# Kernel tuning notes

Measured on AMD Instinct MI355X. Metric: run time of the kernel, lower is better.

The kernel has to match this reference:

```python
import jax, jax.numpy as jnp
import numpy as np

N = 100000
D = 256
E = 300000


def setup_inputs() -> dict:
    key = jax.random.key(0)
    ks = jax.random.split(key, 9)
    x_all = jax.random.normal(ks[0], (N, D), dtype=jnp.float32)
    edge_index = jax.random.randint(ks[1], (2, E), 0, N, dtype=jnp.int64)
    s = 1.0 / np.sqrt(D)
    params = {}
    for i, layer in enumerate(["1", "2", "3"]):
        params[f"Wl{layer}"] = jax.random.uniform(ks[2 + 2 * i], (D, D), jnp.float32, -s, s)
        params[f"Wr{layer}"] = jax.random.uniform(ks[3 + 2 * i], (D, D), jnp.float32, -s, s)
        params[f"b{layer}"] = jnp.zeros((D,), jnp.float32)
    return {"edge_index": edge_index, "x_all": x_all, **params}


def sage_conv(x, src, dst, Wl, Wr, b):
    # PyG SAGEConv: lin_l(mean_{j in N(i)} x_j) + lin_r(x_i), bias on lin_l
    msgs = x[src]                                        # [E, D] gather
    agg = jax.ops.segment_sum(msgs, dst, num_segments=N)  # [N, D]
    deg = jax.ops.segment_sum(jnp.ones((src.shape[0],), x.dtype), dst, num_segments=N)
    agg = agg / jnp.maximum(deg, 1.0)[:, None]           # mean; isolated nodes -> 0
    return agg @ Wl.T + x @ Wr.T + b


def reference(edge_index, x_all, Wl1, Wr1, b1, Wl2, Wr2, b2, Wl3, Wr3, b3):
    src, dst = edge_index[0], edge_index[1]
    x = jax.nn.relu(sage_conv(x_all, src, dst, Wl1, Wr1, b1))
    # dropout p=0.4 is identity at inference (training=False)
    x = jax.nn.relu(sage_conv(x, src, dst, Wl2, Wr2, b2))
    x = sage_conv(x, src, dst, Wl3, Wr3, b3)
    return x
```

## Files before the change

kernel.cpp:

```cpp
#include <hip/hip_runtime.h>

typedef unsigned short ushort_t;
typedef unsigned int   u32;
typedef __attribute__((ext_vector_type(8))) short bf16x8;
typedef __attribute__((ext_vector_type(4))) float f32x4;

#define NNODES 100000
#define DIM    256
#define NEDGE  300000
#define KTOT   512
#define KSTEPS 16
#define BROWS  128
#define NTILES 16
#define WCT    8
#define SLICE  16384


__global__ void count_kernel(const int* __restrict__ dst, int* __restrict__ cnt, int E) {
    int e = blockIdx.x * blockDim.x + threadIdx.x;
    if (e < E) atomicAdd(&cnt[dst[e]], 1);
}

__global__ void scan1(const int* __restrict__ cnt, int* __restrict__ partial, int n) {
    __shared__ int s[256];
    int i = blockIdx.x * 256 + threadIdx.x;
    s[threadIdx.x] = (i < n) ? cnt[i] : 0;
    __syncthreads();
    for (int off = 128; off > 0; off >>= 1) {
        if (threadIdx.x < off) s[threadIdx.x] += s[threadIdx.x + off];
        __syncthreads();
    }
    if (threadIdx.x == 0) partial[blockIdx.x] = s[0];
}

__global__ void scan2(int* __restrict__ partial, int nb) {
    __shared__ int s[512];
    int t = threadIdx.x;
    int orig = (t < nb) ? partial[t] : 0;
    s[t] = orig;
    __syncthreads();
    for (int off = 1; off < 512; off <<= 1) {
        int v = (t >= off) ? s[t - off] : 0;
        __syncthreads();
        s[t] += v;
        __syncthreads();
    }
    if (t < nb) partial[t] = s[t] - orig;
}

__global__ void scan3(const int* __restrict__ cnt, const int* __restrict__ partial,
                      int* __restrict__ row_start, int n) {
    __shared__ int s[256];
    int i = blockIdx.x * 256 + threadIdx.x;
    int v = (i < n) ? cnt[i] : 0;
    s[threadIdx.x] = v;
    __syncthreads();
    for (int off = 1; off < 256; off <<= 1) {
        int t = (threadIdx.x >= off) ? s[threadIdx.x - off] : 0;
        __syncthreads();
        s[threadIdx.x] += t;
        __syncthreads();
    }
    if (i < n) row_start[i] = partial[blockIdx.x] + s[threadIdx.x] - v;
}

__global__ void fill_csr(const int* __restrict__ src, const int* __restrict__ dst,
                         const int* __restrict__ row_start, int* __restrict__ cursor,
                         int* __restrict__ esrc, int E) {
    int e = blockIdx.x * blockDim.x + threadIdx.x;
    if (e < E) {
        int d = dst[e];
        int pos = row_start[d] + atomicAdd(&cursor[d], 1);
        esrc[pos] = src[e];
    }
}

__global__ __launch_bounds__(256) void aggregate(
    const int* __restrict__ esrc, const int* __restrict__ row_start,
    const int* __restrict__ cnt, const float* __restrict__ x, float* __restrict__ agg)
{
    int node = (blockIdx.x * blockDim.x + threadIdx.x) >> 6;
    int lane = threadIdx.x & 63;
    if (node >= NNODES) return;
    int start = row_start[node];
    int c = cnt[node];
    float4 acc = make_float4(0.f, 0.f, 0.f, 0.f);
    for (int i = 0; i < c; i++) {
        int s = esrc[start + i];
        float4 v = ((const float4*)(x + (size_t)s * DIM))[lane];
        acc.x += v.x; acc.y += v.y; acc.z += v.z; acc.w += v.w;
    }
    float inv = (c > 0) ? 1.0f / (float)c : 0.0f;
    ((float4*)(agg + (size_t)node * DIM))[lane] =
        make_float4(acc.x * inv, acc.y * inv, acc.z * inv, acc.w * inv);
}

__global__ void conv_weights(const float* __restrict__ Wl, const float* __restrict__ Wr,
                             ushort_t* __restrict__ Bsw) {
    int idx = blockIdx.x * 256 + threadIdx.x;
    if (idx >= 256 * KTOT) return;
    int n = idx >> 9, k = idx & 511;
    float v = (k < DIM) ? Wl[n * DIM + k] : Wr[n * DIM + (k - DIM)];
    unsigned u = __float_as_uint(v);
    unsigned hb = u & 0xFFFF0000u;
    float lo = v - __uint_as_float(hb);
    int ks = k >> 5, q = (k >> 3) & 3, j = k & 7;
    int ct = n >> 4, nn = n & 15;
    int base = ks * SLICE + ct * 512 + q * 128 + nn * 8 + j;
    Bsw[base]        = (ushort_t)(u >> 16);
    Bsw[base + 8192] = (ushort_t)(__float_as_uint(lo) >> 16);
}


__device__ __forceinline__ void stage_b_async(const ushort_t* __restrict__ slice,
                                              ushort_t* buf, int tid) {
    const int wave = tid >> 6;
    #pragma unroll
    for (int i = 0; i < 4; i++) {
        const int c  = tid + i * 512;
        const int cb = wave * 64 + i * 512;
        __builtin_amdgcn_global_load_lds(
            (const __attribute__((address_space(1))) u32*)(slice + (size_t)c * 8),
            (__attribute__((address_space(3))) u32*)(buf + cb * 8),
            16, 0, 0);
    }
}

__device__ __forceinline__ void load_a(const float* __restrict__ base, int row0, int row1,
                                       int kk, int M, float* va ) {
    if (row0 < M) {
        *(float4*)(va + 0) = *(const float4*)(base + (size_t)row0 * DIM + kk);
        *(float4*)(va + 4) = *(const float4*)(base + (size_t)row0 * DIM + kk + 4);
    } else {
        *(float4*)(va + 0) = make_float4(0.f, 0.f, 0.f, 0.f);
        *(float4*)(va + 4) = make_float4(0.f, 0.f, 0.f, 0.f);
    }
    if (row1 < M) {
        *(float4*)(va + 8)  = *(const float4*)(base + (size_t)row1 * DIM + kk);
        *(float4*)(va + 12) = *(const float4*)(base + (size_t)row1 * DIM + kk + 4);
    } else {
        *(float4*)(va + 8)  = make_float4(0.f, 0.f, 0.f, 0.f);
        *(float4*)(va + 12) = make_float4(0.f, 0.f, 0.f, 0.f);
    }
}

__device__ __forceinline__ void split8(const float* __restrict__ a, bf16x8& h, bf16x8& l) {
    #pragma unroll
    for (int i = 0; i < 8; i++) {
        float x = a[i];
        unsigned u = __float_as_uint(x);
        unsigned hb = u & 0xFFFF0000u;
        h[i] = (short)(u >> 16);
        float lo = x - __uint_as_float(hb);
        l[i] = (short)(__float_as_uint(lo) >> 16);
    }
}

__global__ __launch_bounds__(512, 4) void sage_gemm_mfma(
    const float* __restrict__ agg, const float* __restrict__ xin,
    const ushort_t* __restrict__ Bsw,
    const float* __restrict__ bias, float* __restrict__ out, int M, int do_relu)
{
    __shared__ __align__(16) ushort_t Bs[2][SLICE];

    const int tid  = threadIdx.x;
    const int lane = tid & 63;
    const int wave = tid >> 6;
    const int lrow = lane & 15;
    const int quad = lane >> 4;
    const int rg   = wave >> 1;
    const int cg   = wave & 1;

    const int rowbase = blockIdx.x * BROWS + rg * 32;
    const int arow0 = rowbase + lrow;
    const int arow1 = rowbase + 16 + lrow;
    const int kq    = quad * 8;
    const int ctbase = cg * WCT;

    f32x4 acc[2][WCT];
    #pragma unroll
    for (int i = 0; i < 2; i++)
        #pragma unroll
        for (int j = 0; j < WCT; j++)
            acc[i][j] = (f32x4){0.f, 0.f, 0.f, 0.f};

    float aN[16];
    stage_b_async(Bsw, &Bs[0][0], tid);
    load_a(agg, arow0, arow1, kq, M, aN);

    for (int ks = 0; ks < KSTEPS; ks++) {
        __syncthreads();
        if (ks + 1 < KSTEPS)
            stage_b_async(Bsw + (size_t)(ks + 1) * SLICE, &Bs[(ks + 1) & 1][0], tid);

        bf16x8 ah0, al0, ah1, al1;
        split8(aN + 0, ah0, al0);
        split8(aN + 8, ah1, al1);

        if (ks + 1 < KSTEPS) {
            int ks1 = ks + 1;
            const float* base = (ks1 < 8) ? agg : xin;
            int kk = ((ks1 < 8) ? ks1 * 32 : (ks1 - 8) * 32) + kq;
            load_a(base, arow0, arow1, kk, M, aN);
        }

        const ushort_t* bp = &Bs[ks & 1][ctbase * 512 + lane * 8];
        #pragma unroll
        for (int j = 0; j < WCT; j++) {
            const bf16x8 bh = *(const bf16x8*)(bp + j * 512);
            const bf16x8 bl = *(const bf16x8*)(bp + 8192 + j * 512);
            acc[0][j] = __builtin_amdgcn_mfma_f32_16x16x32_bf16(ah0, bh, acc[0][j], 0, 0, 0);
            acc[1][j] = __builtin_amdgcn_mfma_f32_16x16x32_bf16(ah1, bh, acc[1][j], 0, 0, 0);
            acc[0][j] = __builtin_amdgcn_mfma_f32_16x16x32_bf16(al0, bh, acc[0][j], 0, 0, 0);
            acc[1][j] = __builtin_amdgcn_mfma_f32_16x16x32_bf16(al1, bh, acc[1][j], 0, 0, 0);
            acc[0][j] = __builtin_amdgcn_mfma_f32_16x16x32_bf16(ah0, bl, acc[0][j], 0, 0, 0);
            acc[1][j] = __builtin_amdgcn_mfma_f32_16x16x32_bf16(ah1, bl, acc[1][j], 0, 0, 0);
        }
    }

    #pragma unroll
    for (int j = 0; j < WCT; j++) {
        const int col = (ctbase + j) * 16 + lrow;
        const float bv = bias[col];
        #pragma unroll
        for (int rt = 0; rt < 2; rt++) {
            const int row = rowbase + rt * 16 + quad * 4;
            #pragma unroll
            for (int r = 0; r < 4; r++) {
                if (row + r < M) {
                    float v = acc[rt][j][r] + bv;
                    if (do_relu) v = fmaxf(v, 0.f);
                    out[(size_t)(row + r) * DIM + col] = v;
                }
            }
        }
    }
}

extern "C" void kernel_launch(void* const* d_in, const int* in_sizes, int n_in,
                              void* d_out, int out_size, void* d_ws, size_t ws_size,
                              hipStream_t stream) {
    const int*   edge = (const int*)d_in[0];
    const int*   src  = edge;
    const int*   dst  = edge + NEDGE;
    const float* x    = (const float*)d_in[1];
    const float* Wl1  = (const float*)d_in[2];
    const float* Wr1  = (const float*)d_in[3];
    const float* b1   = (const float*)d_in[4];
    const float* Wl2  = (const float*)d_in[5];
    const float* Wr2  = (const float*)d_in[6];
    const float* b2   = (const float*)d_in[7];
    const float* Wl3  = (const float*)d_in[8];
    const float* Wr3  = (const float*)d_in[9];
    const float* b3   = (const float*)d_in[10];

    const size_t feat = (size_t)NNODES * DIM;
    float*    agg       = (float*)d_ws;
    float*    h2        = agg + feat;
    int*      cnt       = (int*)(h2 + feat);
    int*      row_start = cnt + NNODES;
    int*      cursor    = row_start + NNODES;
    int*      partial   = cursor + NNODES;
    int*      esrc      = partial + 512;
    ushort_t* Bsw       = (ushort_t*)(esrc + NEDGE);
    float*    h1        = (float*)d_out;

    const int nScanBlocks = (NNODES + 255) / 256;

    hipMemsetAsync(cnt, 0, NNODES * sizeof(int), stream);
    hipMemsetAsync(cursor, 0, NNODES * sizeof(int), stream);
    count_kernel<<<(NEDGE + 255) / 256, 256, 0, stream>>>(dst, cnt, NEDGE);
    scan1<<<nScanBlocks, 256, 0, stream>>>(cnt, partial, NNODES);
    scan2<<<1, 512, 0, stream>>>(partial, nScanBlocks);
    scan3<<<nScanBlocks, 256, 0, stream>>>(cnt, partial, row_start, NNODES);
    fill_csr<<<(NEDGE + 255) / 256, 256, 0, stream>>>(src, dst, row_start, cursor, esrc, NEDGE);

    const int aggBlocks  = (NNODES * 64 + 255) / 256;
    const int gemmBlocks = (NNODES + BROWS - 1) / BROWS;
    const int convBlocks = (256 * KTOT + 255) / 256;

    conv_weights<<<convBlocks, 256, 0, stream>>>(Wl1, Wr1, Bsw);
    aggregate<<<aggBlocks, 256, 0, stream>>>(esrc, row_start, cnt, x, agg);
    sage_gemm_mfma<<<gemmBlocks, 512, 0, stream>>>(agg, x, Bsw, b1, h1, NNODES, 1);

    conv_weights<<<convBlocks, 256, 0, stream>>>(Wl2, Wr2, Bsw);
    aggregate<<<aggBlocks, 256, 0, stream>>>(esrc, row_start, cnt, h1, agg);
    sage_gemm_mfma<<<gemmBlocks, 512, 0, stream>>>(agg, h1, Bsw, b2, h2, NNODES, 1);

    conv_weights<<<convBlocks, 256, 0, stream>>>(Wl3, Wr3, Bsw);
    aggregate<<<aggBlocks, 256, 0, stream>>>(esrc, row_start, cnt, h2, agg);
    sage_gemm_mfma<<<gemmBlocks, 512, 0, stream>>>(agg, h2, Bsw, b3, (float*)d_out, NNODES, 0);
}
```

Measured before the change: 615.4 us.

## Prefetch A two steps ahead with manual waitcnt barriers and permuted K layout

The GEMM now keeps two A register buffers and prefetches the A tile two K-steps ahead. The __syncthreads is replaced by an explicit vmcnt wait plus s_barrier with sched_barriers, and the loop is fully unrolled. The K index permutation in both the weight swizzle and the A loads is changed so each lane reads two float4 spaced 16 apart, which gives more coalesced row segments. Out-of-range rows are clamped rather than branched. The aim is to hide global load latency behind the MFMA work, at the cost of more registers and a fragile hand-counted vmcnt.

```diff
diff --git a/kernel.cpp b/kernel.cpp
--- a/kernel.cpp
+++ b/kernel.cpp
@@ -11,7 +11,6 @@
 #define KTOT   512
 #define KSTEPS 16
 #define BROWS  128
-#define NTILES 16
 #define WCT    8
 #define SLICE  16384
 
@@ -104,7 +103,10 @@
     unsigned u = __float_as_uint(v);
     unsigned hb = u & 0xFFFF0000u;
     float lo = v - __uint_as_float(hb);
-    int ks = k >> 5, q = (k >> 3) & 3, j = k & 7;
+    int ks = k >> 5;
+    int k5 = k & 31;
+    int q  = (k5 >> 2) & 3;
+    int j  = (k5 & 3) | ((k5 >> 4) << 2);
     int ct = n >> 4, nn = n & 15;
     int base = ks * SLICE + ct * 512 + q * 128 + nn * 8 + j;
     Bsw[base]        = (ushort_t)(u >> 16);
@@ -127,21 +129,15 @@
 }
 
 __device__ __forceinline__ void load_a(const float* __restrict__ base, int row0, int row1,
-                                       int kk, int M, float* va ) {
-    if (row0 < M) {
-        *(float4*)(va + 0) = *(const float4*)(base + (size_t)row0 * DIM + kk);
-        *(float4*)(va + 4) = *(const float4*)(base + (size_t)row0 * DIM + kk + 4);
-    } else {
-        *(float4*)(va + 0) = make_float4(0.f, 0.f, 0.f, 0.f);
-        *(float4*)(va + 4) = make_float4(0.f, 0.f, 0.f, 0.f);
-    }
-    if (row1 < M) {
-        *(float4*)(va + 8)  = *(const float4*)(base + (size_t)row1 * DIM + kk);
-        *(float4*)(va + 12) = *(const float4*)(base + (size_t)row1 * DIM + kk + 4);
-    } else {
-        *(float4*)(va + 8)  = make_float4(0.f, 0.f, 0.f, 0.f);
-        *(float4*)(va + 12) = make_float4(0.f, 0.f, 0.f, 0.f);
-    }
+                                       int kk, int q, int M, float* va ) {
+    const int r0 = (row0 < M) ? row0 : (M - 1);
+    const int r1 = (row1 < M) ? row1 : (M - 1);
+    const float* p0 = base + (size_t)r0 * DIM + kk + 4 * q;
+    const float* p1 = base + (size_t)r1 * DIM + kk + 4 * q;
+    *(float4*)(va + 0)  = *(const float4*)(p0);
+    *(float4*)(va + 4)  = *(const float4*)(p0 + 16);
+    *(float4*)(va + 8)  = *(const float4*)(p1);
+    *(float4*)(va + 12) = *(const float4*)(p1 + 16);
 }
 
 __device__ __forceinline__ void split8(const float* __restrict__ a, bf16x8& h, bf16x8& l) {
@@ -174,7 +170,6 @@
     const int rowbase = blockIdx.x * BROWS + rg * 32;
     const int arow0 = rowbase + lrow;
     const int arow1 = rowbase + 16 + lrow;
-    const int kq    = quad * 8;
     const int ctbase = cg * WCT;
 
     f32x4 acc[2][WCT];
@@ -184,24 +179,38 @@
         for (int j = 0; j < WCT; j++)
             acc[i][j] = (f32x4){0.f, 0.f, 0.f, 0.f};
 
-    float aN[16];
+    float a0[16], a1[16];
+
     stage_b_async(Bsw, &Bs[0][0], tid);
-    load_a(agg, arow0, arow1, kq, M, aN);
-
+    load_a(agg, arow0, arow1, 0, quad, M, a0);
+    load_a(agg, arow0, arow1, 32, quad, M, a1);
+
+    #pragma unroll
     for (int ks = 0; ks < KSTEPS; ks++) {
-        __syncthreads();
+        __builtin_amdgcn_sched_barrier(0);
+        if (ks == KSTEPS - 1) {
+            asm volatile("s_waitcnt vmcnt(0)" ::: "memory");
+        } else {
+            asm volatile("s_waitcnt vmcnt(4)" ::: "memory");
+        }
+        __builtin_amdgcn_s_barrier();
+        __builtin_amdgcn_sched_barrier(0);
+
         if (ks + 1 < KSTEPS)
             stage_b_async(Bsw + (size_t)(ks + 1) * SLICE, &Bs[(ks + 1) & 1][0], tid);
+        __builtin_amdgcn_sched_barrier(0);
+
+        float* curA = (ks & 1) ? a1 : a0;
 
         bf16x8 ah0, al0, ah1, al1;
-        split8(aN + 0, ah0, al0);
-        split8(aN + 8, ah1, al1);
-
-        if (ks + 1 < KSTEPS) {
-            int ks1 = ks + 1;
-            const float* base = (ks1 < 8) ? agg : xin;
-            int kk = ((ks1 < 8) ? ks1 * 32 : (ks1 - 8) * 32) + kq;
-            load_a(base, arow0, arow1, kk, M, aN);
+        split8(curA + 0, ah0, al0);
+        split8(curA + 8, ah1, al1);
+
+        if (ks + 2 < KSTEPS) {
+            const int ks2 = ks + 2;
+            const float* basep = (ks2 < 8) ? agg : xin;
+            const int kk = (ks2 < 8) ? ks2 * 32 : (ks2 - 8) * 32;
+            load_a(basep, arow0, arow1, kk, quad, M, curA);
         }
 
         const ushort_t* bp = &Bs[ks & 1][ctbase * 512 + lane * 8];
```

After: 770.8 us. 1.25x slower.
